# Optimization experiments

Measured on AMD Instinct MI355X. Metric: run time of the kernel, lower is better.

The kernel has to match this reference:

```python
import math
import jax, jax.numpy as jnp
import numpy as np

B, S, M, D, H, FF = 2, 2048, 64, 1024, 16, 4096
HD = D // H


def setup_inputs() -> dict:
    key = jax.random.key(0)
    ks = jax.random.split(key, 16)
    w = lambda k, shape: jax.random.normal(k, shape, dtype=jnp.float32) * 0.02
    # RoPE angles: theta_i = pos / 10000^(2i/head_dim)
    inv_freq = 1.0 / (10000.0 ** (jnp.arange(0, HD, 2, dtype=jnp.float32) / HD))
    ang = jnp.arange(S, dtype=jnp.float32)[:, None] * inv_freq[None, :]  # (S, HD//2)
    return {
        "tgt": jax.random.normal(ks[0], (B, S, D), dtype=jnp.float32),
        "memory": jax.random.normal(ks[1], (B, M, D), dtype=jnp.float32),
        "rope_cos": jnp.cos(ang),
        "rope_sin": jnp.sin(ang),
        "W_qkv": w(ks[2], (D, 3 * D)), "b_qkv": jnp.zeros((3 * D,), jnp.float32),
        "W_o": w(ks[3], (D, D)), "b_o": jnp.zeros((D,), jnp.float32),
        "Wq_c": w(ks[4], (D, D)), "bq_c": jnp.zeros((D,), jnp.float32),
        "Wk_c": w(ks[5], (D, D)), "bk_c": jnp.zeros((D,), jnp.float32),
        "Wv_c": w(ks[6], (D, D)), "bv_c": jnp.zeros((D,), jnp.float32),
        "W_co": w(ks[7], (D, D)), "b_co": jnp.zeros((D,), jnp.float32),
        "W1": w(ks[8], (D, FF)), "b1": jnp.zeros((FF,), jnp.float32),
        "W2": w(ks[9], (FF, D)), "b2": jnp.zeros((D,), jnp.float32),
        "g1": jnp.ones((D,), jnp.float32), "be1": jnp.zeros((D,), jnp.float32),
        "g2": jnp.ones((D,), jnp.float32), "be2": jnp.zeros((D,), jnp.float32),
        "g3": jnp.ones((D,), jnp.float32), "be3": jnp.zeros((D,), jnp.float32),
    }


def _layer_norm(x, g, b, eps=1e-5):
    mu = jnp.mean(x, axis=-1, keepdims=True)
    var = jnp.mean(jnp.square(x - mu), axis=-1, keepdims=True)
    return (x - mu) * jax.lax.rsqrt(var + eps) * g + b


def _apply_rope(x, cos, sin):
    # x: (B, H, S, HD); cos/sin: (S, HD//2). Pairs (even, odd) rotated as complex.
    xe, xo = x[..., 0::2], x[..., 1::2]
    c = cos[None, None]
    s = sin[None, None]
    re = xe * c - xo * s
    im = xe * s + xo * c
    return jnp.stack([re, im], axis=-1).reshape(x.shape)


def reference(tgt, memory, rope_cos, rope_sin, W_qkv, b_qkv, W_o, b_o,
              Wq_c, bq_c, Wk_c, bk_c, Wv_c, bv_c, W_co, b_co,
              W1, b1, W2, b2, g1, be1, g2, be2, g3, be3):
    b, s, d = tgt.shape
    scale = 1.0 / math.sqrt(HD)

    # --- RoPE self-attention (causal) ---
    x = _layer_norm(tgt, g1, be1)
    qkv = (x @ W_qkv + b_qkv).reshape(b, s, 3, H, HD)
    qkv = jnp.transpose(qkv, (2, 0, 3, 1, 4))  # (3, b, H, s, HD)
    q, k, v = qkv[0], qkv[1], qkv[2]
    q = _apply_rope(q, rope_cos[:s], rope_sin[:s])
    k = _apply_rope(k, rope_cos[:s], rope_sin[:s])
    attn = jnp.einsum('bhqd,bhkd->bhqk', q, k) * scale
    causal = jnp.tril(jnp.ones((s, s), dtype=bool))
    attn = jnp.where(causal[None, None], attn, -1e9)
    attn = jax.nn.softmax(attn, axis=-1)
    sa = jnp.einsum('bhqk,bhkd->bhqd', attn, v)
    sa = jnp.transpose(sa, (0, 2, 1, 3)).reshape(b, s, d)
    tgt = tgt + (sa @ W_o + b_o)

    # --- cross-attention to memory (no positional encoding) ---
    x = _layer_norm(tgt, g2, be2)
    m = memory.shape[1]
    qc = (x @ Wq_c + bq_c).reshape(b, s, H, HD).transpose(0, 2, 1, 3)
    kc = (memory @ Wk_c + bk_c).reshape(b, m, H, HD).transpose(0, 2, 1, 3)
    vc = (memory @ Wv_c + bv_c).reshape(b, m, H, HD).transpose(0, 2, 1, 3)
    ca = jax.nn.softmax(jnp.einsum('bhqd,bhkd->bhqk', qc, kc) * scale, axis=-1)
    co = jnp.einsum('bhqk,bhkd->bhqd', ca, vc)
    co = jnp.transpose(co, (0, 2, 1, 3)).reshape(b, s, d)
    tgt = tgt + (co @ W_co + b_co)

    # --- FFN (exact GELU, dropout disabled = eval) ---
    x = _layer_norm(tgt, g3, be3)
    ffn = jax.nn.gelu(x @ W1 + b1, approximate=False) @ W2 + b2
    return tgt + ffn
```

## Files before the change

### kernel.cpp

```cpp
#include <hip/hip_runtime.h>

typedef unsigned short u16;
typedef short bf16x8 __attribute__((ext_vector_type(8)));
typedef float f32x4 __attribute__((ext_vector_type(4)));

#define HN 16
#define SD 64
#define SEQ 2048
#define DM 1024
#define QSC 0.18033688f

__device__ __forceinline__ float bf2f(u16 h) {
  return __uint_as_float(((unsigned int)h) << 16);
}
__device__ __forceinline__ u16 f2bf(float f) {
  unsigned int x = __float_as_uint(f);
  x += 0x7fffu + ((x >> 16) & 1u);
  return (u16)(x >> 16);
}
__device__ __forceinline__ float geluf(float x) {
  return 0.5f * x * (1.0f + erff(x * 0.70710678118654752f));
}
__device__ __forceinline__ void load_lds16(const u16* g, u16* l) {
  __builtin_amdgcn_global_load_lds(
      (const __attribute__((address_space(1))) void*)g,
      (__attribute__((address_space(3))) void*)l, 16, 0, 0);
}

__device__ __forceinline__ void trans_tile(const float* __restrict__ in,
                                           u16* __restrict__ out, int K, int N,
                                           int tx, int ty, int tid,
                                           u16 (*T)[72]) {
  const int n0 = tx * 64, k0 = ty * 64;
#pragma unroll
  for (int it = 0; it < 2; ++it) {
    const int t = it * 256 + tid, r = t >> 3, c = (t & 7) * 8;
    const float* src = &in[(size_t)(k0 + r) * N + n0 + c];
    float4 d0 = *(const float4*)src;
    float4 d1 = *(const float4*)(src + 4);
    T[r][c + 0] = f2bf(d0.x);
    T[r][c + 1] = f2bf(d0.y);
    T[r][c + 2] = f2bf(d0.z);
    T[r][c + 3] = f2bf(d0.w);
    T[r][c + 4] = f2bf(d1.x);
    T[r][c + 5] = f2bf(d1.y);
    T[r][c + 6] = f2bf(d1.z);
    T[r][c + 7] = f2bf(d1.w);
  }
  __syncthreads();
#pragma unroll
  for (int it = 0; it < 2; ++it) {
    const int t = it * 256 + tid, r = t >> 3, c = (t & 7) * 8;
    uint4 d;
    u16* p = (u16*)&d;
#pragma unroll
    for (int j = 0; j < 8; ++j) p[j] = T[c + j][r];
    *(uint4*)&out[(size_t)(n0 + r) * K + k0 + c] = d;
  }
}

__global__ __launch_bounds__(256) void prep1(
    const float* __restrict__ Wqkv, const float* __restrict__ Wo,
    const float* __restrict__ Wqc, const float* __restrict__ Wkc,
    const float* __restrict__ Wvc, const float* __restrict__ Wco,
    u16* __restrict__ Tqkv, u16* __restrict__ To, u16* __restrict__ Tqc,
    u16* __restrict__ Tkc, u16* __restrict__ Tvc, u16* __restrict__ Tco,
    const float* __restrict__ mem, u16* __restrict__ memb) {
  __shared__ u16 T[64][72];
  const int t = blockIdx.x, tid = threadIdx.x;
  if (t < 768) {
    trans_tile(Wqkv, Tqkv, 1024, 3072, t % 48, t / 48, tid, T);
    return;
  }
  if (t < 2048) {
    const int u = t - 768, m = u >> 8, sub = u & 255;
    const float* in;
    u16* out;
    if (m == 0) { in = Wo; out = To; }
    else if (m == 1) { in = Wqc; out = Tqc; }
    else if (m == 2) { in = Wkc; out = Tkc; }
    else if (m == 3) { in = Wvc; out = Tvc; }
    else { in = Wco; out = Tco; }
    trans_tile(in, out, 1024, 1024, sub & 15, sub >> 4, tid, T);
    return;
  }
  const int i = ((t - 2048) * 256 + tid) * 4;
  float4 d = *(const float4*)&mem[i];
  uint2 o;
  u16* po = (u16*)&o;
  po[0] = f2bf(d.x);
  po[1] = f2bf(d.y);
  po[2] = f2bf(d.z);
  po[3] = f2bf(d.w);
  *(uint2*)&memb[i] = o;
}

__global__ __launch_bounds__(256) void prep2(const float* __restrict__ W1,
                                             const float* __restrict__ W2,
                                             u16* __restrict__ T1,
                                             u16* __restrict__ T2) {
  __shared__ u16 T[64][72];
  const int t = blockIdx.x, tid = threadIdx.x;
  if (t < 1024) {
    trans_tile(W1, T1, 1024, 4096, t & 63, t >> 6, tid, T);
  } else {
    const int u = t - 1024;
    trans_tile(W2, T2, 4096, 1024, u & 15, u >> 4, tid, T);
  }
}

__global__ __launch_bounds__(256) void ln_kernel(
    const float* __restrict__ x, const float* __restrict__ g,
    const float* __restrict__ be, u16* __restrict__ y) {
  const int row = blockIdx.x, tid = threadIdx.x;
  const float* xr = x + (size_t)row * DM;
  float4 d = *(const float4*)&xr[tid * 4];
  float v[4] = {d.x, d.y, d.z, d.w};
  float s1 = 0.f, s2 = 0.f;
#pragma unroll
  for (int j = 0; j < 4; ++j) {
    s1 += v[j];
    s2 += v[j] * v[j];
  }
#pragma unroll
  for (int dd = 1; dd < 64; dd <<= 1) {
    s1 += __shfl_xor(s1, dd, 64);
    s2 += __shfl_xor(s2, dd, 64);
  }
  __shared__ float p1[4], p2[4];
  const int lane = tid & 63, wv = tid >> 6;
  if (lane == 0) {
    p1[wv] = s1;
    p2[wv] = s2;
  }
  __syncthreads();
  s1 = p1[0] + p1[1] + p1[2] + p1[3];
  s2 = p2[0] + p2[1] + p2[2] + p2[3];
  const float mu = s1 * (1.f / DM);
  const float rs = rsqrtf(fmaxf(s2 * (1.f / DM) - mu * mu, 0.f) + 1e-5f);
  float4 gg = *(const float4*)&g[tid * 4];
  float4 bb = *(const float4*)&be[tid * 4];
  const float gv[4] = {gg.x, gg.y, gg.z, gg.w};
  const float bv[4] = {bb.x, bb.y, bb.z, bb.w};
  uint2 o;
  u16* po = (u16*)&o;
#pragma unroll
  for (int j = 0; j < 4; ++j) po[j] = f2bf((v[j] - mu) * rs * gv[j] + bv[j]);
  *(uint2*)&y[(size_t)row * DM + tid * 4] = o;
}

template <int EPI, int TM>
__global__ __launch_bounds__(256) void gemm_bt(
    const u16* __restrict__ A, const u16* __restrict__ Bt,
    const float* __restrict__ bias, const float* __restrict__ resid,
    void* __restrict__ C0, u16* __restrict__ C1, u16* __restrict__ C2, int M,
    int N, int K, int rpbl, float sc, const float* __restrict__ rcos,
    const float* __restrict__ rsin) {
  constexpr int MI = TM / 32;
  __shared__ __align__(16) u16 As[TM][64];
  __shared__ __align__(16) u16 Bs[128][64];
  const int tid = threadIdx.x;
  const int lane = tid & 63, wv = tid >> 6;
  const int l16 = lane & 15, quad = lane >> 4;

  if (EPI == 6 && blockIdx.z) {
    Bt = (const u16*)C1;
    bias = resid;
  }

  int bx = blockIdx.x, by = blockIdx.y;
  const int gx = gridDim.x, gy = gridDim.y;
  if ((gy & 7) == 0) {
    const int f = by * gx + bx;
    const int c = f & 7, j = f >> 3;
    const int jm = j / gx;
    by = c * (gy >> 3) + jm;
    bx = j - jm * gx;
  }
  const int m0 = by * TM, n0 = bx * 128;
  const int wm = (wv >> 1) * (TM / 2), wn = (wv & 1) * 64;

  const int srow = lane >> 3;
  const int sblk = (lane & 7) ^ srow;
  const u16* ag[MI];
  const u16* bg[4];
  u16* la[MI];
  u16* lb[4];
#pragma unroll
  for (int i = 0; i < MI; ++i) {
    const int r0 = i * 32 + wv * 8;
    ag[i] = A + (size_t)(m0 + r0 + srow) * K + sblk * 8;
    la[i] = &As[r0][0] + lane * 8;
  }
#pragma unroll
  for (int i = 0; i < 4; ++i) {
    const int r0 = i * 32 + wv * 8;
    bg[i] = Bt + (size_t)(n0 + r0 + srow) * K + sblk * 8;
    lb[i] = &Bs[r0][0] + lane * 8;
  }

  f32x4 acc[MI][4] = {};

  for (int k0 = 0; k0 < K; k0 += 64) {
    __syncthreads();
#pragma unroll
    for (int i = 0; i < MI; ++i) load_lds16(ag[i] + k0, la[i]);
#pragma unroll
    for (int i = 0; i < 4; ++i) load_lds16(bg[i] + k0, lb[i]);
    __syncthreads();
#pragma unroll
    for (int kk = 0; kk < 2; ++kk) {
      bf16x8 af[MI], bfr[4];
#pragma unroll
      for (int mi = 0; mi < MI; ++mi) {
        const int row = wm + mi * 16 + l16;
        const int blk = (kk * 4 + quad) ^ (row & 7);
        af[mi] = *(const bf16x8*)&As[row][blk * 8];
      }
#pragma unroll
      for (int ni = 0; ni < 4; ++ni) {
        const int row = wn + ni * 16 + l16;
        const int blk = (kk * 4 + quad) ^ (row & 7);
        bfr[ni] = *(const bf16x8*)&Bs[row][blk * 8];
      }
#pragma unroll
      for (int mi = 0; mi < MI; ++mi)
#pragma unroll
        for (int ni = 0; ni < 4; ++ni)
          acc[mi][ni] = __builtin_amdgcn_mfma_f32_16x16x32_bf16(
              af[mi], bfr[ni], acc[mi][ni], 0, 0, 0);
    }
  }

  const int SL = 1 << rpbl;
#pragma unroll
  for (int mi = 0; mi < MI; ++mi) {
#pragma unroll
    for (int ni = 0; ni < 4; ++ni) {
#pragma unroll
      for (int r = 0; r < 4; ++r) {
        const int row = m0 + wm + mi * 16 + quad * 4 + r;
        const int col = n0 + wn + ni * 16 + l16;
        float vv = acc[mi][ni][r] + bias[col];
        if (EPI == 1) {
          vv += resid[(size_t)row * N + col];
          ((float*)C0)[(size_t)row * N + col] = vv;
        } else if (EPI == 2) {
          ((u16*)C0)[(size_t)row * N + col] = f2bf(geluf(vv));
        } else if (EPI == 3) {
          const float partner = __shfl_xor(vv, 1);
          const int which = col >> 10;
          const int nn = col & 1023;
          const int h = nn >> 6, hd = nn & 63;
          const int b = row >> rpbl;
          const int s = row & (SL - 1);
          if (which == 2) {
            C2[(((size_t)b * HN + h) * SD + hd) * SL + s] = f2bf(vv);
          } else {
            const int p = hd >> 1;
            const float cv = rcos[s * 32 + p];
            const float sv2 = rsin[s * 32 + p];
            float o = (hd & 1) ? (partner * sv2 + vv * cv)
                               : (vv * cv - partner * sv2);
            if (which == 0) o *= QSC;
            u16* dst = (which == 0) ? (u16*)C0 : C1;
            dst[(((size_t)b * HN + h) * SL + s) * SD + hd] = f2bf(o);
          }
        } else if (EPI == 4) {
          vv *= sc;
          const int h = col >> 6, hd = col & 63;
          const int b = row >> rpbl;
          const int s = row & (SL - 1);
          ((u16*)C0)[(((size_t)b * HN + h) * SL + s) * SD + hd] = f2bf(vv);
        } else if (EPI == 5) {
          const int h = col >> 6, hd = col & 63;
          const int b = row >> rpbl;
          const int s = row & (SL - 1);
          ((u16*)C0)[(((size_t)b * HN + h) * SD + hd) * SL + s] = f2bf(vv);
        } else if (EPI == 6) {
          const int h = col >> 6, hd = col & 63;
          const int b = row >> rpbl;
          const int s = row & (SL - 1);
          if (blockIdx.z == 0)
            ((u16*)C0)[(((size_t)b * HN + h) * SL + s) * SD + hd] = f2bf(vv);
          else
            C2[(((size_t)b * HN + h) * SD + hd) * SL + s] = f2bf(vv);
        } else {
          ((u16*)C0)[(size_t)row * N + col] = f2bf(vv);
        }
      }
    }
  }
}

template <int CAUSAL>
__global__ __launch_bounds__(512, 4) void attn_kernel(
    const u16* __restrict__ q, const u16* __restrict__ k,
    const u16* __restrict__ vt, u16* __restrict__ out, int kv_len) {
  __shared__ u16 Qs[128][72], Ks[64][72], VTs[64][72];
  __shared__ u16 Ps[128][68];
  const int tid = threadIdx.x;
  const int lane = tid & 63, wv = tid >> 6;
  const int t2 = wv >> 2, w4 = wv & 3;
  const int l16 = lane & 15, quad = lane >> 4;
  const int bx = blockIdx.x, bh = blockIdx.y;
  const int qtA = bx;
  const int qtB = CAUSAL ? (31 - bx) : (bx + 16);
  const int qt = t2 ? qtB : qtA;
  const u16* qb = q + (size_t)bh * SEQ * SD;
  const u16* kb = k + (size_t)bh * kv_len * SD;
  const u16* vtb = vt + (size_t)bh * SD * kv_len;

#pragma unroll
  for (int it = 0; it < 2; ++it) {
    const int t = it * 512 + tid, r = t >> 3, c = (t & 7) * 8;
    const int qrow = (r < 64) ? (qtA * 64 + r) : (qtB * 64 + (r - 64));
    *(uint4*)&Qs[r][c] = *(const uint4*)&qb[(size_t)qrow * SD + c];
  }

  f32x4 o_acc[4] = {};
  float l_i[4] = {};

  const int ktiles = CAUSAL ? (qtB + 1) : ((kv_len + 63) >> 6);
  const int sr = tid >> 3, sc8 = (tid & 7) * 8;

  for (int kt = 0; kt < ktiles; ++kt) {
    const uint4 kd = *(const uint4*)&kb[((size_t)kt * 64 + sr) * SD + sc8];
    const uint4 vd = *(const uint4*)&vtb[(size_t)sr * kv_len + kt * 64 + sc8];
    __syncthreads();
    *(uint4*)&Ks[sr][sc8] = kd;
    *(uint4*)&VTs[sr][sc8] = vd;
    __syncthreads();

    if (kt <= qt) {
      const int roff = t2 * 64 + w4 * 16;
      f32x4 s_acc[4] = {};
#pragma unroll
      for (int kk = 0; kk < 64; kk += 32) {
        const bf16x8 aq = *(const bf16x8*)&Qs[roff + l16][kk + quad * 8];
#pragma unroll
        for (int ni = 0; ni < 4; ++ni) {
          const bf16x8 bk = *(const bf16x8*)&Ks[ni * 16 + l16][kk + quad * 8];
          s_acc[ni] = __builtin_amdgcn_mfma_f32_16x16x32_bf16(aq, bk, s_acc[ni],
                                                              0, 0, 0);
        }
      }
      float rsum[4] = {0.f, 0.f, 0.f, 0.f};
      const bool dg = CAUSAL && (kt == qt);
#pragma unroll
      for (int ni = 0; ni < 4; ++ni)
#pragma unroll
        for (int r = 0; r < 4; ++r) {
          float sv = s_acc[ni][r];
          if (dg && (ni * 16 + l16 > w4 * 16 + quad * 4 + r)) sv = -1e9f;
          const float pe = __builtin_amdgcn_exp2f(sv);
          rsum[r] += pe;
          Ps[wv * 16 + quad * 4 + r][ni * 16 + l16] =
              (u16)(__float_as_uint(pe) >> 16);
        }
#pragma unroll
      for (int r = 0; r < 4; ++r) {
#pragma unroll
        for (int dd = 1; dd < 16; dd <<= 1)
          rsum[r] += __shfl_xor(rsum[r], dd, 64);
        l_i[r] += rsum[r];
      }
#pragma unroll
      for (int kk = 0; kk < 64; kk += 32) {
        const bf16x8 ap = *(const bf16x8*)&Ps[wv * 16 + l16][kk + quad * 8];
#pragma unroll
        for (int ni = 0; ni < 4; ++ni) {
          const bf16x8 bv = *(const bf16x8*)&VTs[ni * 16 + l16][kk + quad * 8];
          o_acc[ni] = __builtin_amdgcn_mfma_f32_16x16x32_bf16(ap, bv, o_acc[ni],
                                                              0, 0, 0);
        }
      }
    }
  }

  const int b = bh >> 4, h = bh & 15;
#pragma unroll
  for (int r = 0; r < 4; ++r) {
    const float inv = 1.f / l_i[r];
    const int s = qt * 64 + w4 * 16 + quad * 4 + r;
#pragma unroll
    for (int ni = 0; ni < 4; ++ni)
      out[((size_t)b * SEQ + s) * DM + h * SD + ni * 16 + l16] =
          f2bf(o_acc[ni][r] * inv);
  }
}

extern "C" void kernel_launch(void* const* d_in, const int* in_sizes, int n_in,
                              void* d_out, int out_size, void* d_ws,
                              size_t ws_size, hipStream_t stream) {
  (void)in_sizes;
  (void)n_in;
  (void)out_size;
  (void)ws_size;
  const float* tgt = (const float*)d_in[0];
  const float* mem = (const float*)d_in[1];
  const float* rc = (const float*)d_in[2];
  const float* rsn = (const float*)d_in[3];
  const float* W_qkv = (const float*)d_in[4];
  const float* b_qkv = (const float*)d_in[5];
  const float* W_o = (const float*)d_in[6];
  const float* b_o = (const float*)d_in[7];
  const float* Wq_c = (const float*)d_in[8];
  const float* bq_c = (const float*)d_in[9];
  const float* Wk_c = (const float*)d_in[10];
  const float* bk_c = (const float*)d_in[11];
  const float* Wv_c = (const float*)d_in[12];
  const float* bv_c = (const float*)d_in[13];
  const float* W_co = (const float*)d_in[14];
  const float* b_co = (const float*)d_in[15];
  const float* W1 = (const float*)d_in[16];
  const float* b1 = (const float*)d_in[17];
  const float* W2 = (const float*)d_in[18];
  const float* b2 = (const float*)d_in[19];
  const float* g1 = (const float*)d_in[20];
  const float* be1 = (const float*)d_in[21];
  const float* g2 = (const float*)d_in[22];
  const float* be2 = (const float*)d_in[23];
  const float* g3 = (const float*)d_in[24];
  const float* be3 = (const float*)d_in[25];

  const size_t M1 = 1048576;
  u16* w = (u16*)d_ws;
  u16* WTqkv = w;
  u16* WTo = w + 3 * M1;
  u16* WTqc = w + 4 * M1;
  u16* WTkc = w + 5 * M1;
  u16* WTvc = w + 6 * M1;
  u16* WTco = w + 7 * M1;
  u16* WT1 = w;
  u16* WT2 = w + 4 * M1;
  u16* xb = w + 8 * M1;
  u16* qb = w + 12 * M1;
  u16* kb = w + 16 * M1;
  u16* vbT = w + 20 * M1;
  u16* at = w + 24 * M1;
  u16* kc = w + 28 * M1;
  u16* vcT = kc + 131072;
  u16* memb = vcT + 131072;
  u16* ffh = qb;
  float* res = (float*)d_out;

  dim3 blk(256), blk512(512);
  prep1<<<2176, blk, 0, stream>>>(W_qkv, W_o, Wq_c, Wk_c, Wv_c, W_co, WTqkv,
                                  WTo, WTqc, WTkc, WTvc, WTco, mem, memb);

  ln_kernel<<<4096, blk, 0, stream>>>(tgt, g1, be1, xb);
  gemm_bt<3, 128><<<dim3(24, 32), blk, 0, stream>>>(
      xb, WTqkv, b_qkv, nullptr, qb, kb, vbT, 4096, 3072, 1024, 11, 1.f, rc,
      rsn);
  attn_kernel<1><<<dim3(16, 32), blk512, 0, stream>>>(qb, kb, vbT, at, 2048);
  gemm_bt<1, 64><<<dim3(8, 64), blk, 0, stream>>>(at, WTo, b_o, tgt, res,
                                                  nullptr, nullptr, 4096, 1024,
                                                  1024, 0, 1.f, nullptr,
                                                  nullptr);
  ln_kernel<<<4096, blk, 0, stream>>>(res, g2, be2, xb);
  gemm_bt<4, 64><<<dim3(8, 64), blk, 0, stream>>>(
      xb, WTqc, bq_c, nullptr, qb, nullptr, nullptr, 4096, 1024, 1024, 11, QSC,
      nullptr, nullptr);
  gemm_bt<6, 64><<<dim3(8, 2, 2), blk, 0, stream>>>(
      memb, WTkc, bk_c, bv_c, kc, WTvc, vcT, 128, 1024, 1024, 6, 1.f, nullptr,
      nullptr);
  attn_kernel<0><<<dim3(16, 32), blk512, 0, stream>>>(qb, kc, vcT, at, 64);
  gemm_bt<1, 64><<<dim3(8, 64), blk, 0, stream>>>(at, WTco, b_co, res, res,
                                                  nullptr, nullptr, 4096, 1024,
                                                  1024, 0, 1.f, nullptr,
                                                  nullptr);
  prep2<<<2048, blk, 0, stream>>>(W1, W2, WT1, WT2);
  ln_kernel<<<4096, blk, 0, stream>>>(res, g3, be3, xb);
  gemm_bt<2, 128><<<dim3(32, 32), blk, 0, stream>>>(
      xb, WT1, b1, nullptr, ffh, nullptr, nullptr, 4096, 4096, 1024, 0, 1.f,
      nullptr, nullptr);
  gemm_bt<1, 64><<<dim3(8, 64), blk, 0, stream>>>(ffh, WT2, b2, res, res,
                                                  nullptr, nullptr, 4096, 1024,
                                                  4096, 0, 1.f, nullptr,
                                                  nullptr);
}
```

Before: 515.9 us.

## Double-buffer GEMM LDS tiles and rotate K start per block

The GEMM kernel now allocates two LDS buffers for the A and B tiles. It issues the async global-to-LDS load for the next K slice before computing the current one, which removes one barrier per iteration and overlaps loads with MFMA work. Each block also starts its K loop at an offset derived from its tile coordinates, to spread concurrent reads across K. The cost is doubled LDS use, which may lower occupancy, and the staggered start assumes K/64 is a power of two.

```diff
diff --git a/kernel.cpp b/kernel.cpp
--- a/kernel.cpp
+++ b/kernel.cpp
@@ -157,8 +157,8 @@
     int N, int K, int rpbl, float sc, const float* __restrict__ rcos,
     const float* __restrict__ rsin) {
   constexpr int MI = TM / 32;
-  __shared__ __align__(16) u16 As[TM][64];
-  __shared__ __align__(16) u16 Bs[128][64];
+  __shared__ __align__(16) u16 As[2 * TM * 64];
+  __shared__ __align__(16) u16 Bs[2 * 128 * 64];
   const int tid = threadIdx.x;
   const int lane = tid & 63, wv = tid >> 6;
   const int l16 = lane & 15, quad = lane >> 4;
@@ -190,24 +190,26 @@
   for (int i = 0; i < MI; ++i) {
     const int r0 = i * 32 + wv * 8;
     ag[i] = A + (size_t)(m0 + r0 + srow) * K + sblk * 8;
-    la[i] = &As[r0][0] + lane * 8;
+    la[i] = As + r0 * 64 + lane * 8;
   }
 #pragma unroll
   for (int i = 0; i < 4; ++i) {
     const int r0 = i * 32 + wv * 8;
     bg[i] = Bt + (size_t)(n0 + r0 + srow) * K + sblk * 8;
-    lb[i] = &Bs[r0][0] + lane * 8;
+    lb[i] = Bs + r0 * 64 + lane * 8;
   }
 
   f32x4 acc[MI][4] = {};
 
-  for (int k0 = 0; k0 < K; k0 += 64) {
-    __syncthreads();
-#pragma unroll
-    for (int i = 0; i < MI; ++i) load_lds16(ag[i] + k0, la[i]);
-#pragma unroll
-    for (int i = 0; i < 4; ++i) load_lds16(bg[i] + k0, lb[i]);
-    __syncthreads();
+  auto stage = [&](int cb, int k0) {
+#pragma unroll
+    for (int i = 0; i < MI; ++i) load_lds16(ag[i] + k0, la[i] + cb * (TM * 64));
+#pragma unroll
+    for (int i = 0; i < 4; ++i) load_lds16(bg[i] + k0, lb[i] + cb * (128 * 64));
+  };
+  auto compute = [&](int cb) {
+    const u16* Ab = As + cb * (TM * 64);
+    const u16* Bb = Bs + cb * (128 * 64);
 #pragma unroll
     for (int kk = 0; kk < 2; ++kk) {
       bf16x8 af[MI], bfr[4];
@@ -215,13 +217,13 @@
       for (int mi = 0; mi < MI; ++mi) {
         const int row = wm + mi * 16 + l16;
         const int blk = (kk * 4 + quad) ^ (row & 7);
-        af[mi] = *(const bf16x8*)&As[row][blk * 8];
+        af[mi] = *(const bf16x8*)&Ab[row * 64 + blk * 8];
       }
 #pragma unroll
       for (int ni = 0; ni < 4; ++ni) {
         const int row = wn + ni * 16 + l16;
         const int blk = (kk * 4 + quad) ^ (row & 7);
-        bfr[ni] = *(const bf16x8*)&Bs[row][blk * 8];
+        bfr[ni] = *(const bf16x8*)&Bb[row * 64 + blk * 8];
       }
 #pragma unroll
       for (int mi = 0; mi < MI; ++mi)
@@ -230,7 +232,23 @@
           acc[mi][ni] = __builtin_amdgcn_mfma_f32_16x16x32_bf16(
               af[mi], bfr[ni], acc[mi][ni], 0, 0, 0);
     }
-  }
+  };
+
+  const int nk = K >> 6;
+  int s = (bx + by) & (nk - 1);
+  stage(0, s << 6);
+  __syncthreads();
+  int cur = 0;
+  for (int t = 1; t < nk; ++t) {
+    int sn = s + 1;
+    if (sn == nk) sn = 0;
+    stage(cur ^ 1, sn << 6);
+    compute(cur);
+    __syncthreads();
+    cur ^= 1;
+    s = sn;
+  }
+  compute(cur);
 
   const int SL = 1 << rpbl;
 #pragma unroll
@@ -253,38 +271,38 @@
           const int nn = col & 1023;
           const int h = nn >> 6, hd = nn & 63;
           const int b = row >> rpbl;
-          const int s = row & (SL - 1);
+          const int s2 = row & (SL - 1);
           if (which == 2) {
-            C2[(((size_t)b * HN + h) * SD + hd) * SL + s] = f2bf(vv);
+            C2[(((size_t)b * HN + h) * SD + hd) * SL + s2] = f2bf(vv);
           } else {
             const int p = hd >> 1;
-            const float cv = rcos[s * 32 + p];
-            const float sv2 = rsin[s * 32 + p];
+            const float cv = rcos[s2 * 32 + p];
+            const float sv2 = rsin[s2 * 32 + p];
             float o = (hd & 1) ? (partner * sv2 + vv * cv)
                                : (vv * cv - partner * sv2);
             if (which == 0) o *= QSC;
             u16* dst = (which == 0) ? (u16*)C0 : C1;
-            dst[(((size_t)b * HN + h) * SL + s) * SD + hd] = f2bf(o);
+            dst[(((size_t)b * HN + h) * SL + s2) * SD + hd] = f2bf(o);
           }
         } else if (EPI == 4) {
           vv *= sc;
           const int h = col >> 6, hd = col & 63;
           const int b = row >> rpbl;
-          const int s = row & (SL - 1);
-          ((u16*)C0)[(((size_t)b * HN + h) * SL + s) * SD + hd] = f2bf(vv);
+          const int s2 = row & (SL - 1);
+          ((u16*)C0)[(((size_t)b * HN + h) * SL + s2) * SD + hd] = f2bf(vv);
         } else if (EPI == 5) {
           const int h = col >> 6, hd = col & 63;
           const int b = row >> rpbl;
-          const int s = row & (SL - 1);
-          ((u16*)C0)[(((size_t)b * HN + h) * SD + hd) * SL + s] = f2bf(vv);
+          const int s2 = row & (SL - 1);
+          ((u16*)C0)[(((size_t)b * HN + h) * SD + hd) * SL + s2] = f2bf(vv);
         } else if (EPI == 6) {
           const int h = col >> 6, hd = col & 63;
           const int b = row >> rpbl;
-          const int s = row & (SL - 1);
+          const int s2 = row & (SL - 1);
           if (blockIdx.z == 0)
-            ((u16*)C0)[(((size_t)b * HN + h) * SL + s) * SD + hd] = f2bf(vv);
+            ((u16*)C0)[(((size_t)b * HN + h) * SL + s2) * SD + hd] = f2bf(vv);
           else
-            C2[(((size_t)b * HN + h) * SD + hd) * SL + s] = f2bf(vv);
+            C2[(((size_t)b * HN + h) * SD + hd) * SL + s2] = f2bf(vv);
         } else {
           ((u16*)C0)[(size_t)row * N + col] = f2bf(vv);
         }
```

Result: no change. 518.6 us (+0.5%).

## Add 256x256 8-wave pipelined GEMM for QKV and FFN-up projections

Applied to the files above, without the earlier changes.

Introduces a new GEMM kernel with 256x256 tiles, 512 threads, swizzled LDS layout, and a four-phase software pipeline that interleaves global-to-LDS loads with MFMA work, using setprio and barriers. It replaces the 128-tile GEMM for the QKV projection (with RoPE epilogue) and the FFN first layer (GELU epilogue). The aim is better data reuse and overlap of memory with compute on the two largest GEMMs. In exchange the grids get smaller (192 and 256 blocks), which may underfill the CUs, and register pressure rises.

```diff
diff --git a/kernel.cpp b/kernel.cpp
--- a/kernel.cpp
+++ b/kernel.cpp
@@ -293,6 +293,131 @@
   }
 }
 
+template <int EPI>
+__global__ __launch_bounds__(512, 2) void gemm8p(
+    const u16* __restrict__ A, const u16* __restrict__ Bt,
+    const float* __restrict__ bias, void* __restrict__ C0,
+    u16* __restrict__ C1, u16* __restrict__ C2, int M, int N, int K, int rpbl,
+    const float* __restrict__ rcos, const float* __restrict__ rsin) {
+  __shared__ __align__(16) u16 L[4][2][8192];
+  const int tid = threadIdx.x;
+  const int lane = tid & 63, wv = tid >> 6;
+  const int l16 = lane & 15, quad = lane >> 4;
+  const int bx = blockIdx.x, by = blockIdx.y;
+  const int m0 = by * 256, n0 = bx * 256;
+  const int wm = (wv >> 2) * 128, wn = (wv & 3) * 64;
+  const int nk = K >> 6;
+
+  const u16* Ag = A + (size_t)m0 * K;
+  const u16* Bg = Bt + (size_t)n0 * K;
+
+  auto stage = [&](int mat, int h, int st) {
+    const int tt = st < nk ? st : nk - 1;
+    const int k0 = tt << 6;
+    u16* dst = &L[mat * 2 + h][st & 1][0];
+    const u16* src = mat ? Bg : Ag;
+#pragma unroll
+    for (int j = 0; j < 2; ++j) {
+      const int li = wv * 2 + j;
+      const int p = li * 8 + (lane >> 3);
+      const int b = lane & 7;
+      const int g = b ^ (p & 7);
+      const int row = 2 * p + (g >> 2);
+      load_lds16(src + (size_t)row * K + k0 + h * 32 + (g & 3) * 8,
+                 dst + li * 512 + lane * 8);
+    }
+  };
+
+  f32x4 acc[8][4] = {};
+  bf16x8 bfr[4];
+
+#define PHASE(CB, KK, MH, RB, SM, SH, ST, VM)                                \
+  {                                                                          \
+    const u16* Ar = &L[KK][CB][0];                                           \
+    const u16* Br = &L[2 + KK][CB][0];                                       \
+    bf16x8 af[4];                                                            \
+    _Pragma("unroll") for (int mi = 0; mi < 4; ++mi) {                       \
+      const int R = wm + MH * 64 + mi * 16 + l16;                            \
+      const int p = R >> 1, g = (R & 1) * 4 + quad, b = g ^ (p & 7);         \
+      af[mi] = *(const bf16x8*)&Ar[p * 64 + b * 8];                          \
+    }                                                                        \
+    if (RB) {                                                                \
+      _Pragma("unroll") for (int ni = 0; ni < 4; ++ni) {                     \
+        const int R = wn + ni * 16 + l16;                                    \
+        const int p = R >> 1, g = (R & 1) * 4 + quad, b = g ^ (p & 7);       \
+        bfr[ni] = *(const bf16x8*)&Br[p * 64 + b * 8];                       \
+      }                                                                      \
+    }                                                                        \
+    stage(SM, SH, ST);                                                       \
+    __builtin_amdgcn_s_barrier();                                            \
+    asm volatile("s_waitcnt lgkmcnt(0)" ::: "memory");                       \
+    __builtin_amdgcn_s_setprio(1);                                           \
+    _Pragma("unroll") for (int mi = 0; mi < 4; ++mi)                         \
+        _Pragma("unroll") for (int ni = 0; ni < 4; ++ni) acc[MH * 4 + mi]    \
+            [ni] = __builtin_amdgcn_mfma_f32_16x16x32_bf16(                  \
+                af[mi], bfr[ni], acc[MH * 4 + mi][ni], 0, 0, 0);             \
+    __builtin_amdgcn_s_setprio(0);                                           \
+    if (VM) asm volatile("s_waitcnt vmcnt(8)" ::: "memory");                 \
+    __builtin_amdgcn_s_barrier();                                            \
+  }
+
+  stage(0, 0, 0);
+  stage(1, 0, 0);
+  stage(0, 1, 0);
+  stage(1, 1, 0);
+  stage(0, 0, 1);
+  stage(1, 0, 1);
+  asm volatile("s_waitcnt vmcnt(8)" ::: "memory");
+  __builtin_amdgcn_s_barrier();
+
+  for (int t = 0; t < nk; ++t) {
+    const int cb = t & 1;
+    PHASE(cb, 0, 0, true, 0, 1, t + 1, false)
+    PHASE(cb, 0, 1, false, 1, 1, t + 1, true)
+    PHASE(cb, 1, 0, true, 0, 0, t + 2, false)
+    PHASE(cb, 1, 1, false, 1, 0, t + 2, true)
+  }
+#undef PHASE
+
+  const int SL = 1 << rpbl;
+#pragma unroll
+  for (int mi = 0; mi < 8; ++mi) {
+#pragma unroll
+    for (int ni = 0; ni < 4; ++ni) {
+#pragma unroll
+      for (int r = 0; r < 4; ++r) {
+        const int row = m0 + wm + mi * 16 + quad * 4 + r;
+        const int col = n0 + wn + ni * 16 + l16;
+        float vv = acc[mi][ni][r] + bias[col];
+        if (EPI == 2) {
+          ((u16*)C0)[(size_t)row * N + col] = f2bf(geluf(vv));
+        } else if (EPI == 3) {
+          const float partner = __shfl_xor(vv, 1);
+          const int which = col >> 10;
+          const int nn = col & 1023;
+          const int h = nn >> 6, hd = nn & 63;
+          const int b = row >> rpbl;
+          const int s = row & (SL - 1);
+          if (which == 2) {
+            C2[(((size_t)b * HN + h) * SD + hd) * SL + s] = f2bf(vv);
+          } else {
+            const int p = hd >> 1;
+            const float cv = rcos[s * 32 + p];
+            const float sv2 = rsin[s * 32 + p];
+            float o = (hd & 1) ? (partner * sv2 + vv * cv)
+                               : (vv * cv - partner * sv2);
+            if (which == 0) o *= QSC;
+            u16* dst = (which == 0) ? (u16*)C0 : C1;
+            dst[(((size_t)b * HN + h) * SL + s) * SD + hd] = f2bf(o);
+          }
+        } else {
+          ((u16*)C0)[(size_t)row * N + col] = f2bf(vv);
+        }
+      }
+    }
+  }
+}
+
 template <int CAUSAL>
 __global__ __launch_bounds__(512, 4) void attn_kernel(
     const u16* __restrict__ q, const u16* __restrict__ k,
@@ -450,9 +575,8 @@
                                   WTo, WTqc, WTkc, WTvc, WTco, mem, memb);
 
   ln_kernel<<<4096, blk, 0, stream>>>(tgt, g1, be1, xb);
-  gemm_bt<3, 128><<<dim3(24, 32), blk, 0, stream>>>(
-      xb, WTqkv, b_qkv, nullptr, qb, kb, vbT, 4096, 3072, 1024, 11, 1.f, rc,
-      rsn);
+  gemm8p<3><<<dim3(12, 16), blk512, 0, stream>>>(xb, WTqkv, b_qkv, qb, kb, vbT,
+                                                 4096, 3072, 1024, 11, rc, rsn);
   attn_kernel<1><<<dim3(16, 32), blk512, 0, stream>>>(qb, kb, vbT, at, 2048);
   gemm_bt<1, 64><<<dim3(8, 64), blk, 0, stream>>>(at, WTo, b_o, tgt, res,
                                                   nullptr, nullptr, 4096, 1024,
@@ -472,9 +596,9 @@
                                                   nullptr);
   prep2<<<2048, blk, 0, stream>>>(W1, W2, WT1, WT2);
   ln_kernel<<<4096, blk, 0, stream>>>(res, g3, be3, xb);
-  gemm_bt<2, 128><<<dim3(32, 32), blk, 0, stream>>>(
-      xb, WT1, b1, nullptr, ffh, nullptr, nullptr, 4096, 4096, 1024, 0, 1.f,
-      nullptr, nullptr);
+  gemm8p<2><<<dim3(16, 16), blk512, 0, stream>>>(xb, WT1, b1, ffh, nullptr,
+                                                 nullptr, 4096, 4096, 1024, 0,
+                                                 nullptr, nullptr);
   gemm_bt<1, 64><<<dim3(8, 64), blk, 0, stream>>>(ffh, WT2, b2, res, res,
                                                   nullptr, nullptr, 4096, 1024,
                                                   4096, 0, 1.f, nullptr,
```

Measured after the change: 490.3 us. 1.05x faster.

## Double-buffer GEMM LDS tiles and swizzle/prefetch attention K/V tiles

Applied to the files above, without the earlier changes.

The GEMM kernel now keeps two LDS buffers and issues the next K-tile's global-to-LDS loads before computing on the current one. It uses precomputed LDS addresses, inline ds_read_b128 and raised wave priority around the MFMA block, so each tile needs one barrier instead of two. The attention kernel replaces padded LDS rows with XOR-swizzled layouts, prefetches the next K/V tile into registers during compute, and remaps blocks to group heads for cache locality. This doubles GEMM LDS use, which may lower occupancy. The inline asm waitcnt scheduling is fragile, and the last stage loads a clamped duplicate tile.

```diff
diff --git a/kernel.cpp b/kernel.cpp
--- a/kernel.cpp
+++ b/kernel.cpp
@@ -25,6 +25,10 @@
   __builtin_amdgcn_global_load_lds(
       (const __attribute__((address_space(1))) void*)g,
       (__attribute__((address_space(3))) void*)l, 16, 0, 0);
+}
+__device__ __forceinline__ unsigned ldsoff(const u16* p) {
+  return (unsigned)(unsigned long long)(
+      const __attribute__((address_space(3))) u16*)p;
 }
 
 __device__ __forceinline__ void trans_tile(const float* __restrict__ in,
@@ -157,8 +161,8 @@
     int N, int K, int rpbl, float sc, const float* __restrict__ rcos,
     const float* __restrict__ rsin) {
   constexpr int MI = TM / 32;
-  __shared__ __align__(16) u16 As[TM][64];
-  __shared__ __align__(16) u16 Bs[128][64];
+  __shared__ __align__(16) u16 As[2][TM][64];
+  __shared__ __align__(16) u16 Bs[2][128][64];
   const int tid = threadIdx.x;
   const int lane = tid & 63, wv = tid >> 6;
   const int l16 = lane & 15, quad = lane >> 4;
@@ -179,6 +183,7 @@
   }
   const int m0 = by * TM, n0 = bx * 128;
   const int wm = (wv >> 1) * (TM / 2), wn = (wv & 1) * 64;
+  const int nk = K >> 6;
 
   const int srow = lane >> 3;
   const int sblk = (lane & 7) ^ srow;
@@ -190,47 +195,80 @@
   for (int i = 0; i < MI; ++i) {
     const int r0 = i * 32 + wv * 8;
     ag[i] = A + (size_t)(m0 + r0 + srow) * K + sblk * 8;
-    la[i] = &As[r0][0] + lane * 8;
+    la[i] = &As[0][r0][0] + lane * 8;
   }
 #pragma unroll
   for (int i = 0; i < 4; ++i) {
     const int r0 = i * 32 + wv * 8;
     bg[i] = Bt + (size_t)(n0 + r0 + srow) * K + sblk * 8;
-    lb[i] = &Bs[r0][0] + lane * 8;
+    lb[i] = &Bs[0][r0][0] + lane * 8;
+  }
+
+  unsigned aad[2][MI], bad[2][4];
+#pragma unroll
+  for (int kk = 0; kk < 2; ++kk) {
+#pragma unroll
+    for (int mi = 0; mi < MI; ++mi) {
+      const int row = wm + mi * 16 + l16;
+      const int blk = (kk * 4 + quad) ^ (row & 7);
+      aad[kk][mi] = ldsoff(&As[0][0][0]) + (unsigned)(row * 128 + blk * 16);
+    }
+#pragma unroll
+    for (int ni = 0; ni < 4; ++ni) {
+      const int row = wn + ni * 16 + l16;
+      const int blk = (kk * 4 + quad) ^ (row & 7);
+      bad[kk][ni] = ldsoff(&Bs[0][0][0]) + (unsigned)(row * 128 + blk * 16);
+    }
   }
 
   f32x4 acc[MI][4] = {};
 
-  for (int k0 = 0; k0 < K; k0 += 64) {
-    __syncthreads();
-#pragma unroll
-    for (int i = 0; i < MI; ++i) load_lds16(ag[i] + k0, la[i]);
-#pragma unroll
-    for (int i = 0; i < 4; ++i) load_lds16(bg[i] + k0, lb[i]);
-    __syncthreads();
-#pragma unroll
-    for (int kk = 0; kk < 2; ++kk) {
-      bf16x8 af[MI], bfr[4];
-#pragma unroll
-      for (int mi = 0; mi < MI; ++mi) {
-        const int row = wm + mi * 16 + l16;
-        const int blk = (kk * 4 + quad) ^ (row & 7);
-        af[mi] = *(const bf16x8*)&As[row][blk * 8];
-      }
-#pragma unroll
-      for (int ni = 0; ni < 4; ++ni) {
-        const int row = wn + ni * 16 + l16;
-        const int blk = (kk * 4 + quad) ^ (row & 7);
-        bfr[ni] = *(const bf16x8*)&Bs[row][blk * 8];
-      }
-#pragma unroll
-      for (int mi = 0; mi < MI; ++mi)
-#pragma unroll
-        for (int ni = 0; ni < 4; ++ni)
-          acc[mi][ni] = __builtin_amdgcn_mfma_f32_16x16x32_bf16(
-              af[mi], bfr[ni], acc[mi][ni], 0, 0, 0);
-    }
-  }
+#define STB(P, ST)                                                            \
+  {                                                                           \
+    const int tt = (ST) < nk ? (ST) : nk - 1;                                 \
+    const int k0s = tt << 6;                                                  \
+    _Pragma("unroll") for (int i = 0; i < MI; ++i)                            \
+        load_lds16(ag[i] + k0s, la[i] + (P) * (TM * 64));                     \
+    _Pragma("unroll") for (int i = 0; i < 4; ++i)                             \
+        load_lds16(bg[i] + k0s, lb[i] + (P) * 8192);                          \
+  }
+
+#define TILEB(CB, NP, ST)                                                     \
+  {                                                                           \
+    STB(NP, ST);                                                              \
+    bf16x8 afr[2][MI], bfr[2][4];                                             \
+    _Pragma("unroll") for (int kk = 0; kk < 2; ++kk) {                        \
+      _Pragma("unroll") for (int mi = 0; mi < MI; ++mi)                       \
+          asm volatile("ds_read_b128 %0, %1 offset:%2"                        \
+                       : "=v"(afr[kk][mi])                                    \
+                       : "v"(aad[kk][mi]), "i"((CB) * (TM * 128)));           \
+      _Pragma("unroll") for (int ni = 0; ni < 4; ++ni)                        \
+          asm volatile("ds_read_b128 %0, %1 offset:%2"                        \
+                       : "=v"(bfr[kk][ni])                                    \
+                       : "v"(bad[kk][ni]), "i"((CB)*16384));                  \
+    }                                                                         \
+    asm volatile("s_waitcnt lgkmcnt(0)");                                     \
+    __builtin_amdgcn_sched_barrier(0);                                        \
+    __builtin_amdgcn_s_setprio(1);                                            \
+    _Pragma("unroll") for (int kk = 0; kk < 2; ++kk)                          \
+        _Pragma("unroll") for (int mi = 0; mi < MI; ++mi)                     \
+            _Pragma("unroll") for (int ni = 0; ni < 4; ++ni) acc[mi][ni] =    \
+                __builtin_amdgcn_mfma_f32_16x16x32_bf16(                      \
+                    afr[kk][mi], bfr[kk][ni], acc[mi][ni], 0, 0, 0);          \
+    __builtin_amdgcn_s_setprio(0);                                            \
+    asm volatile("s_waitcnt vmcnt(0)");                                       \
+    __builtin_amdgcn_s_barrier();                                             \
+  }
+
+  STB(0, 0);
+  asm volatile("s_waitcnt vmcnt(0)");
+  __builtin_amdgcn_s_barrier();
+  for (int t = 0; t < nk; t += 2) {
+    TILEB(0, 1, t + 1)
+    TILEB(1, 0, t + 2)
+  }
+#undef TILEB
+#undef STB
 
   const int SL = 1 << rpbl;
 #pragma unroll
@@ -297,13 +335,19 @@
 __global__ __launch_bounds__(512, 4) void attn_kernel(
     const u16* __restrict__ q, const u16* __restrict__ k,
     const u16* __restrict__ vt, u16* __restrict__ out, int kv_len) {
-  __shared__ u16 Qs[128][72], Ks[64][72], VTs[64][72];
-  __shared__ u16 Ps[128][68];
+  __shared__ __align__(16) u16 Qs[128][64], Ks[64][64], VTs[64][64];
+  __shared__ __align__(16) u16 Ps[128][64];
   const int tid = threadIdx.x;
   const int lane = tid & 63, wv = tid >> 6;
   const int t2 = wv >> 2, w4 = wv & 3;
   const int l16 = lane & 15, quad = lane >> 4;
-  const int bx = blockIdx.x, bh = blockIdx.y;
+  int bx, bh;
+  {
+    const int l = blockIdx.y * 16 + blockIdx.x;
+    const int c = l & 7, j = l >> 3;
+    bh = c + 8 * (j >> 4);
+    bx = j & 15;
+  }
   const int qtA = bx;
   const int qtB = CAUSAL ? (31 - bx) : (bx + 16);
   const int qt = t2 ? qtB : qtA;
@@ -313,34 +357,45 @@
 
 #pragma unroll
   for (int it = 0; it < 2; ++it) {
-    const int t = it * 512 + tid, r = t >> 3, c = (t & 7) * 8;
+    const int t = it * 512 + tid, r = t >> 3, cb = t & 7;
     const int qrow = (r < 64) ? (qtA * 64 + r) : (qtB * 64 + (r - 64));
-    *(uint4*)&Qs[r][c] = *(const uint4*)&qb[(size_t)qrow * SD + c];
+    *(uint4*)&Qs[r][(cb ^ (r & 7)) * 8] =
+        *(const uint4*)&qb[(size_t)qrow * SD + cb * 8];
   }
 
   f32x4 o_acc[4] = {};
   float l_i[4] = {};
 
   const int ktiles = CAUSAL ? (qtB + 1) : ((kv_len + 63) >> 6);
-  const int sr = tid >> 3, sc8 = (tid & 7) * 8;
+  const int sr = tid >> 3, scb = tid & 7;
+  const int swb = (scb ^ (sr & 7)) * 8;
+
+  uint4 kd = *(const uint4*)&kb[(size_t)sr * SD + scb * 8];
+  uint4 vd = *(const uint4*)&vtb[(size_t)sr * kv_len + scb * 8];
 
   for (int kt = 0; kt < ktiles; ++kt) {
-    const uint4 kd = *(const uint4*)&kb[((size_t)kt * 64 + sr) * SD + sc8];
-    const uint4 vd = *(const uint4*)&vtb[(size_t)sr * kv_len + kt * 64 + sc8];
     __syncthreads();
-    *(uint4*)&Ks[sr][sc8] = kd;
-    *(uint4*)&VTs[sr][sc8] = vd;
+    *(uint4*)&Ks[sr][swb] = kd;
+    *(uint4*)&VTs[sr][swb] = vd;
     __syncthreads();
+    if (kt + 1 < ktiles) {
+      kd = *(const uint4*)&kb[((size_t)(kt + 1) * 64 + sr) * SD + scb * 8];
+      vd = *(const uint4*)&vtb[(size_t)sr * kv_len + (kt + 1) * 64 + scb * 8];
+    }
 
     if (kt <= qt) {
       const int roff = t2 * 64 + w4 * 16;
+      const int qrw = roff + l16;
       f32x4 s_acc[4] = {};
 #pragma unroll
-      for (int kk = 0; kk < 64; kk += 32) {
-        const bf16x8 aq = *(const bf16x8*)&Qs[roff + l16][kk + quad * 8];
+      for (int kk = 0; kk < 2; ++kk) {
+        const bf16x8 aq =
+            *(const bf16x8*)&Qs[qrw][((kk * 4 + quad) ^ (qrw & 7)) * 8];
 #pragma unroll
         for (int ni = 0; ni < 4; ++ni) {
-          const bf16x8 bk = *(const bf16x8*)&Ks[ni * 16 + l16][kk + quad * 8];
+          const int krw = ni * 16 + l16;
+          const bf16x8 bk =
+              *(const bf16x8*)&Ks[krw][((kk * 4 + quad) ^ (krw & 7)) * 8];
           s_acc[ni] = __builtin_amdgcn_mfma_f32_16x16x32_bf16(aq, bk, s_acc[ni],
                                                               0, 0, 0);
         }
@@ -348,16 +403,19 @@
       float rsum[4] = {0.f, 0.f, 0.f, 0.f};
       const bool dg = CAUSAL && (kt == qt);
 #pragma unroll
-      for (int ni = 0; ni < 4; ++ni)
+      for (int ni = 0; ni < 4; ++ni) {
+        const int colb = ni * 2 + (l16 >> 3);
 #pragma unroll
         for (int r = 0; r < 4; ++r) {
           float sv = s_acc[ni][r];
           if (dg && (ni * 16 + l16 > w4 * 16 + quad * 4 + r)) sv = -1e9f;
           const float pe = __builtin_amdgcn_exp2f(sv);
           rsum[r] += pe;
-          Ps[wv * 16 + quad * 4 + r][ni * 16 + l16] =
+          const int prow = wv * 16 + quad * 4 + r;
+          Ps[prow][((colb ^ (prow & 7)) * 8) + (l16 & 7)] =
               (u16)(__float_as_uint(pe) >> 16);
         }
+      }
 #pragma unroll
       for (int r = 0; r < 4; ++r) {
 #pragma unroll
@@ -365,12 +423,16 @@
           rsum[r] += __shfl_xor(rsum[r], dd, 64);
         l_i[r] += rsum[r];
       }
-#pragma unroll
-      for (int kk = 0; kk < 64; kk += 32) {
-        const bf16x8 ap = *(const bf16x8*)&Ps[wv * 16 + l16][kk + quad * 8];
+      const int prw = wv * 16 + l16;
+#pragma unroll
+      for (int kk = 0; kk < 2; ++kk) {
+        const bf16x8 ap =
+            *(const bf16x8*)&Ps[prw][((kk * 4 + quad) ^ (prw & 7)) * 8];
 #pragma unroll
         for (int ni = 0; ni < 4; ++ni) {
-          const bf16x8 bv = *(const bf16x8*)&VTs[ni * 16 + l16][kk + quad * 8];
+          const int vrw = ni * 16 + l16;
+          const bf16x8 bv =
+              *(const bf16x8*)&VTs[vrw][((kk * 4 + quad) ^ (vrw & 7)) * 8];
           o_acc[ni] = __builtin_amdgcn_mfma_f32_16x16x32_bf16(ap, bv, o_acc[ni],
                                                               0, 0, 0);
         }
```

Measured after the change: 516.4 us. About the same (+0.1%).
